# Kernel tuning notes

Measured on AMD Instinct MI355X. Metric: run time of the kernel, lower is better.

Reference implementation:

```python
import jax, jax.numpy as jnp
import numpy as np

B, T, C, I = 4, 4096, 1024, 4096

def rmsnorm(x, w, eps=1e-6):
    return x * jax.lax.rsqrt(jnp.mean(x * x, axis=-1, keepdims=True) + eps) * w

def shift(h):
    # prepend zeros, drop last timestep: (B,T,C)
    return jnp.pad(h, ((0, 0), (1, 0), (0, 0)))[:, :-1]

def wkv_scan(k, v, w, u):
    # k, v: (B,T,C) fp32; w, u: (C,)
    ew = jnp.exp(jnp.clip(w, -20.0, 20.0))
    def step(carry, kv):
        a, b = carry
        kt, vt = kv  # (B,C)
        ekt = jnp.exp(jnp.clip(u + kt, -20.0, 20.0))
        out = (a + ekt * vt) / (b + ekt + 1e-8)
        ek = jnp.exp(jnp.clip(kt, -20.0, 20.0))
        return (ew * a + ek * vt, ew * b + ek), out
    init = (jnp.zeros((k.shape[0], k.shape[2]), jnp.float32),
            jnp.zeros((k.shape[0], k.shape[2]), jnp.float32))
    _, out = jax.lax.scan(step, init, (k.swapaxes(0, 1), v.swapaxes(0, 1)))
    return out.swapaxes(0, 1)  # (B,T,C)

def setup_inputs() -> dict:
    key = jax.random.key(0)
    ks = jax.random.split(key, 16)
    s = 1.0 / np.sqrt(C)
    si = 1.0 / np.sqrt(I)
    return {
        "x": jax.random.normal(ks[0], (B, T, C), jnp.float32),
        "ln1_w": jnp.ones((C,), jnp.float32),
        "ln2_w": jnp.ones((C,), jnp.float32),
        "time_decay": jax.random.normal(ks[1], (C,), jnp.float32) * 0.1 - 5.0,
        "time_first": jax.random.normal(ks[2], (C,), jnp.float32) * 0.01,
        "time_mix_k": jnp.full((C,), 0.5, jnp.float32),
        "time_mix_v": jnp.full((C,), 0.5, jnp.float32),
        "time_mix_r": jnp.full((C,), 0.5, jnp.float32),
        "W_key": jax.random.normal(ks[3], (C, C), jnp.float32) * s,
        "W_value": jax.random.normal(ks[4], (C, C), jnp.float32) * s,
        "W_recept": jax.random.normal(ks[5], (C, C), jnp.float32) * s,
        "W_out": jax.random.normal(ks[6], (C, C), jnp.float32) * s,
        "time_mix_k2": jnp.full((C,), 0.5, jnp.float32),
        "time_mix_r2": jnp.full((C,), 0.5, jnp.float32),
        "W_key2": jax.random.normal(ks[7], (C, I), jnp.float32) * s,
        "W_value2": jax.random.normal(ks[8], (I, C), jnp.float32) * si,
        "W_recept2": jax.random.normal(ks[9], (C, C), jnp.float32) * s,
    }

def reference(x, ln1_w, ln2_w, time_decay, time_first,
              time_mix_k, time_mix_v, time_mix_r,
              W_key, W_value, W_recept, W_out,
              time_mix_k2, time_mix_r2, W_key2, W_value2, W_recept2):
    # --- time mixing ---
    h = rmsnorm(x, ln1_w)
    sh = shift(h)
    xk = h * time_mix_k + sh * (1 - time_mix_k)
    xv = h * time_mix_v + sh * (1 - time_mix_v)
    xr = h * time_mix_r + sh * (1 - time_mix_r)
    k = xk @ W_key
    v = xv @ W_value
    r = jax.nn.sigmoid(xr @ W_recept)
    w = -jnp.exp(time_decay)
    u = time_first
    wkv = wkv_scan(k.astype(jnp.float32), v.astype(jnp.float32), w, u).astype(x.dtype)
    x = x + (r * wkv) @ W_out
    # --- channel mixing ---
    h = rmsnorm(x, ln2_w)
    sh = shift(h)
    xk = h * time_mix_k2 + sh * (1 - time_mix_k2)
    xr = h * time_mix_r2 + sh * (1 - time_mix_r2)
    k2 = jnp.square(jax.nn.relu(xk @ W_key2))
    r2 = jax.nn.sigmoid(xr @ W_recept2)
    return x + r2 * (k2 @ W_value2)
```

## Files before the change

kernel.cpp:

```cpp
#include <hip/hip_runtime.h>
#include <cstdint>
#include <cstddef>

#define B_ 4
#define T_ 4096
#define C_ 1024
#define I_ 4096
#define M_ (B_*T_)

__device__ __forceinline__ float bf2f(uint16_t u) {
    union { uint32_t i; float f; } v; v.i = ((uint32_t)u) << 16; return v.f;
}
__device__ __forceinline__ uint16_t f2bf(float f) {
    union { float f; uint32_t i; } v; v.f = f;
    uint32_t i = v.i;
    return (uint16_t)((i + 0x7fffu + ((i >> 16) & 1u)) >> 16);
}

typedef __bf16 bf16x8 __attribute__((ext_vector_type(8)));
typedef float  f32x4  __attribute__((ext_vector_type(4)));
typedef uint32_t u32x4 __attribute__((ext_vector_type(4)));

__device__ __forceinline__ void async16(const void* g, void* l) {
    __builtin_amdgcn_global_load_lds(
        (const __attribute__((address_space(1))) void*)g,
        (__attribute__((address_space(3))) void*)l, 16, 0, 0);
}

#define MEMBAR asm volatile("" ::: "memory")
#define BAR    __builtin_amdgcn_s_barrier()

__global__ void sniff_kernel(const uint32_t* __restrict__ w,
                             int* __restrict__ flag, int* __restrict__ one) {
    *flag = (w[0] == 0x3F003F00u) ? 1 : 0;
    *one = 1;
}

struct VecPtrs { const void* s[9]; uint16_t* d[9]; };
__global__ __launch_bounds__(256) void convert_vecs(VecPtrs p, const int* __restrict__ flagp) {
    const int f = *flagp;
    const int tid = threadIdx.x;
    for (int a = 0; a < 9; ++a) {
        const void* s = p.s[a]; uint16_t* d = p.d[a];
        for (int i = tid; i < C_; i += 256)
            d[i] = f ? ((const uint16_t*)s)[i] : f2bf(((const float*)s)[i]);
    }
}

struct TJobs { const void* src[7]; uint16_t* dst[7]; };
__global__ __launch_bounds__(256) void transpose_all(TJobs tj, const int* __restrict__ flagp)
{
    __shared__ uint16_t tile[64][65];
    const int f = *flagp;
    const int bid = blockIdx.x;
    int w, t, R, Cc, cx, cy;
    if (bid < 1280) {
        w = bid >> 8; t = bid & 255; R = C_; Cc = C_; cx = t & 15; cy = t >> 4;
    } else if (bid < 2304) {
        w = 5; t = bid - 1280; R = C_; Cc = I_; cx = t & 63; cy = t >> 6;
    } else {
        w = 6; t = bid - 2304; R = I_; Cc = C_; cx = t & 15; cy = t >> 4;
    }
    const void* in = tj.src[w];
    uint16_t* out = tj.dst[w];
    const int lc = threadIdx.x & 63;
    const int rg = threadIdx.x >> 6;
    const int c0 = cx * 64, r0 = cy * 64;
    #pragma unroll
    for (int i = 0; i < 16; ++i) {
        int lr = rg * 16 + i;
        size_t idx = (size_t)(r0 + lr) * Cc + c0 + lc;
        tile[lr][lc] = f ? ((const uint16_t*)in)[idx] : f2bf(((const float*)in)[idx]);
    }
    __syncthreads();
    #pragma unroll
    for (int i = 0; i < 16; ++i) {
        int lcc = rg * 16 + i;
        out[(size_t)(c0 + lcc) * R + r0 + lc] = tile[lc][lcc];
    }
}

__global__ __launch_bounds__(256) void mix_kernel(
    const void* __restrict__ x, const uint16_t* __restrict__ ln,
    const uint16_t* __restrict__ mk, const uint16_t* __restrict__ mv,
    const uint16_t* __restrict__ mr, const int* __restrict__ flagp,
    uint16_t* __restrict__ xk, uint16_t* __restrict__ xv, uint16_t* __restrict__ xr)
{
    const int row = blockIdx.x;
    const int tid = threadIdx.x;
    const int f = *flagp;
    const bool hasPrev = (row & (T_ - 1)) != 0;
    const size_t base = (size_t)row * C_;

    float c[4], p[4];
    if (f) {
        const uint16_t* xb = (const uint16_t*)x;
        uint2 cu = ((const uint2*)(xb + base))[tid];
        uint2 pu; pu.x = 0u; pu.y = 0u;
        if (hasPrev) pu = ((const uint2*)(xb + base - C_))[tid];
        c[0] = bf2f((uint16_t)(cu.x & 0xffff)); c[1] = bf2f((uint16_t)(cu.x >> 16));
        c[2] = bf2f((uint16_t)(cu.y & 0xffff)); c[3] = bf2f((uint16_t)(cu.y >> 16));
        p[0] = bf2f((uint16_t)(pu.x & 0xffff)); p[1] = bf2f((uint16_t)(pu.x >> 16));
        p[2] = bf2f((uint16_t)(pu.y & 0xffff)); p[3] = bf2f((uint16_t)(pu.y >> 16));
    } else {
        const float* xf = (const float*)x;
        float4 cf = ((const float4*)(xf + base))[tid];
        float4 pf; pf.x = pf.y = pf.z = pf.w = 0.f;
        if (hasPrev) pf = ((const float4*)(xf + base - C_))[tid];
        c[0] = cf.x; c[1] = cf.y; c[2] = cf.z; c[3] = cf.w;
        p[0] = pf.x; p[1] = pf.y; p[2] = pf.z; p[3] = pf.w;
    }

    float s1 = c[0]*c[0] + c[1]*c[1] + c[2]*c[2] + c[3]*c[3];
    float s2 = p[0]*p[0] + p[1]*p[1] + p[2]*p[2] + p[3]*p[3];
    #pragma unroll
    for (int off = 32; off > 0; off >>= 1) {
        s1 += __shfl_down(s1, off);
        s2 += __shfl_down(s2, off);
    }
    __shared__ float red[8];
    const int lane = tid & 63, wave = tid >> 6;
    if (lane == 0) { red[wave * 2] = s1; red[wave * 2 + 1] = s2; }
    __syncthreads();
    s1 = red[0] + red[2] + red[4] + red[6];
    s2 = red[1] + red[3] + red[5] + red[7];
    const float rs1 = rsqrtf(s1 * (1.f / C_) + 1e-6f);
    const float rs2 = rsqrtf(s2 * (1.f / C_) + 1e-6f);

    uint2 lnu = ((const uint2*)ln)[tid];
    uint2 mku = ((const uint2*)mk)[tid];
    uint2 mru = ((const uint2*)mr)[tid];
    float lnv[4] = { bf2f((uint16_t)(lnu.x & 0xffff)), bf2f((uint16_t)(lnu.x >> 16)),
                     bf2f((uint16_t)(lnu.y & 0xffff)), bf2f((uint16_t)(lnu.y >> 16)) };
    float mkv[4] = { bf2f((uint16_t)(mku.x & 0xffff)), bf2f((uint16_t)(mku.x >> 16)),
                     bf2f((uint16_t)(mku.y & 0xffff)), bf2f((uint16_t)(mku.y >> 16)) };
    float mrv[4] = { bf2f((uint16_t)(mru.x & 0xffff)), bf2f((uint16_t)(mru.x >> 16)),
                     bf2f((uint16_t)(mru.y & 0xffff)), bf2f((uint16_t)(mru.y >> 16)) };

    float h[4], sh[4];
    #pragma unroll
    for (int e = 0; e < 4; ++e) {
        h[e]  = c[e] * rs1 * lnv[e];
        sh[e] = p[e] * rs2 * lnv[e];
    }

    uint16_t ok[4], orr[4];
    #pragma unroll
    for (int e = 0; e < 4; ++e) {
        ok[e]  = f2bf(h[e] * mkv[e] + sh[e] * (1.f - mkv[e]));
        orr[e] = f2bf(h[e] * mrv[e] + sh[e] * (1.f - mrv[e]));
    }
    uint2 w;
    w.x = (uint32_t)ok[0] | ((uint32_t)ok[1] << 16);  w.y = (uint32_t)ok[2] | ((uint32_t)ok[3] << 16);
    ((uint2*)(xk + base))[tid] = w;
    w.x = (uint32_t)orr[0] | ((uint32_t)orr[1] << 16); w.y = (uint32_t)orr[2] | ((uint32_t)orr[3] << 16);
    ((uint2*)(xr + base))[tid] = w;

    if (xv != nullptr) {
        uint2 mvu = ((const uint2*)mv)[tid];
        float mvv[4] = { bf2f((uint16_t)(mvu.x & 0xffff)), bf2f((uint16_t)(mvu.x >> 16)),
                         bf2f((uint16_t)(mvu.y & 0xffff)), bf2f((uint16_t)(mvu.y >> 16)) };
        uint16_t ov[4];
        #pragma unroll
        for (int e = 0; e < 4; ++e)
            ov[e] = f2bf(h[e] * mvv[e] + sh[e] * (1.f - mvv[e]));
        w.x = (uint32_t)ov[0] | ((uint32_t)ov[1] << 16);  w.y = (uint32_t)ov[2] | ((uint32_t)ov[3] << 16);
        ((uint2*)(xv + base))[tid] = w;
    }
}

#define SCAN_L   64
#define SCAN_NCH (T_ / SCAN_L)

__global__ __launch_bounds__(256) void wkv_pass1(
    const uint16_t* __restrict__ kb, const uint16_t* __restrict__ vb,
    const uint16_t* __restrict__ td,
    float* __restrict__ sumA, float* __restrict__ sumB)
{
    const int gid = blockIdx.x * 256 + threadIdx.x;
    const int c = gid & (C_ - 1);
    const int j = (gid >> 10) & (SCAN_NCH - 1);
    const int b = gid >> 16;
    float w = -__expf(bf2f(td[c]));
    w = fminf(fmaxf(w, -20.f), 20.f);
    const float ew = __expf(w);
    const size_t base = ((size_t)(b * T_ + j * SCAN_L)) * C_ + c;
    float A = 0.f, Bs = 0.f;
    #pragma unroll 8
    for (int i = 0; i < SCAN_L; ++i) {
        float kt = bf2f(kb[base + (size_t)i * C_]);
        float vt = bf2f(vb[base + (size_t)i * C_]);
        float ek = __expf(fminf(fmaxf(kt, -20.f), 20.f));
        A  = ew * A  + ek * vt;
        Bs = ew * Bs + ek;
    }
    const size_t sidx = ((size_t)(b * SCAN_NCH + j)) * C_ + c;
    sumA[sidx] = A; sumB[sidx] = Bs;
}

__global__ __launch_bounds__(256) void wkv_pass2(
    const float* __restrict__ sumA, const float* __restrict__ sumB,
    const uint16_t* __restrict__ td,
    float* __restrict__ a0s, float* __restrict__ b0s)
{
    const int gid = blockIdx.x * 256 + threadIdx.x;
    const int c = gid & (C_ - 1);
    const int b = gid >> 10;
    float w = -__expf(bf2f(td[c]));
    w = fminf(fmaxf(w, -20.f), 20.f);
    const float dL = __expf(w * (float)SCAN_L);
    float a = 0.f, bs = 0.f;
    for (int j = 0; j < SCAN_NCH; ++j) {
        size_t idx = ((size_t)(b * SCAN_NCH + j)) * C_ + c;
        a0s[idx] = a; b0s[idx] = bs;
        a  = dL * a  + sumA[idx];
        bs = dL * bs + sumB[idx];
    }
}

__global__ __launch_bounds__(256) void wkv_pass3(
    const uint16_t* __restrict__ kb, const uint16_t* __restrict__ vb,
    const uint16_t* __restrict__ rb, const uint16_t* __restrict__ td,
    const uint16_t* __restrict__ tf,
    const float* __restrict__ a0s, const float* __restrict__ b0s,
    uint16_t* __restrict__ rwkv)
{
    const int gid = blockIdx.x * 256 + threadIdx.x;
    const int c = gid & (C_ - 1);
    const int j = (gid >> 10) & (SCAN_NCH - 1);
    const int b = gid >> 16;
    float w = -__expf(bf2f(td[c]));
    w = fminf(fmaxf(w, -20.f), 20.f);
    const float ew = __expf(w);
    const float u = bf2f(tf[c]);
    const size_t base = ((size_t)(b * T_ + j * SCAN_L)) * C_ + c;
    const size_t sidx = ((size_t)(b * SCAN_NCH + j)) * C_ + c;
    float a = a0s[sidx], bs = b0s[sidx];
    #pragma unroll 4
    for (int i = 0; i < SCAN_L; ++i) {
        float kt = bf2f(kb[base + (size_t)i * C_]);
        float vt = bf2f(vb[base + (size_t)i * C_]);
        float rt = bf2f(rb[base + (size_t)i * C_]);
        float eu = __expf(fminf(fmaxf(u + kt, -20.f), 20.f));
        float out = __fdividef(a + eu * vt, bs + eu + 1e-8f);
        rwkv[base + (size_t)i * C_] = f2bf(rt * out);
        float ek = __expf(fminf(fmaxf(kt, -20.f), 20.f));
        a  = ew * a  + ek * vt;
        bs = ew * bs + ek;
    }
}


struct GJob {
    const uint16_t* A; const uint16_t* BT; void* Out;
    const void* aux1; const void* aux2;
    int mode; int N; int K;
};
struct GJobs { GJob j[3]; };

#define EP_PITCH 72
#define EP_QUAD  4608

#define MFMA_QUAD(RB)                                                         \
    _Pragma("unroll")                                                         \
    for (int ii = 0; ii < 4; ++ii) {                                          \
        _Pragma("unroll")                                                     \
        for (int jj = 0; jj < 4; ++jj)                                        \
            acc[(RB) + ii][jj] = __builtin_amdgcn_mfma_f32_16x16x32_bf16(     \
                av[ii], bv[jj], acc[(RB) + ii][jj], 0, 0, 0);                 \
    }

__device__ __forceinline__ void gemm_loop256(
    const uint16_t* __restrict__ Abase, const uint16_t* __restrict__ Bbase,
    const int K, uint16_t* __restrict__ sA, uint16_t* __restrict__ sB,
    const int tid, const int aOff, const int bOff, f32x4 (&acc)[8][4])
{
    const int r0  = tid >> 2;
    const int kg8 = ((tid & 3) ^ ((r0 >> 1) & 3)) * 8;
    const uint16_t* gA = Abase + (size_t)r0 * K + kg8;
    const uint16_t* gB = Bbase + (size_t)r0 * K + kg8;
    uint16_t* dA = sA + tid * 8;
    uint16_t* dB = sB + tid * 8;
    const size_t qs = (size_t)128 * K;
    const int NT = K >> 6;

    async16(gA,      dA);         async16(gA + qs,      dA + 4096);
    async16(gB,      dB);         async16(gB + qs,      dB + 4096);
    async16(gA + 32, dA + 8192);  async16(gA + 32 + qs, dA + 12288);
    async16(gB + 32, dB + 8192);  async16(gB + 32 + qs, dB + 12288);
    asm volatile("s_waitcnt vmcnt(4)" ::: "memory");
    BAR; MEMBAR;

    for (int t = 0; t < NT; ++t) {
        const int s0 = (t & 1) * 2;
        const int n0 = s0 ^ 2;
        const uint16_t* A0 = sA + s0 * 8192 + aOff;
        const uint16_t* B0 = sB + s0 * 8192 + bOff;
        const uint16_t* A1 = A0 + 8192;
        const uint16_t* B1 = B0 + 8192;
        uint16_t* dAn = dA + n0 * 8192;
        uint16_t* dBn = dB + n0 * 8192;
        const bool pf = (t + 1 < NT);
        const int ko = (t + 1) << 6;
        bf16x8 av[4], bv[4];

        #pragma unroll
        for (int ii = 0; ii < 4; ++ii) av[ii] = *(const bf16x8*)(A0 + ii * 512);
        #pragma unroll
        for (int jj = 0; jj < 4; ++jj) bv[jj] = *(const bf16x8*)(B0 + jj * 512);
        if (pf) {
            async16(gA + ko,      dAn);          async16(gA + ko + qs,      dAn + 4096);
            async16(gB + ko,      dBn);          async16(gB + ko + qs,      dBn + 4096);
            async16(gA + ko + 32, dAn + 8192);   async16(gA + ko + 32 + qs, dAn + 12288);
            async16(gB + ko + 32, dBn + 8192);   async16(gB + ko + 32 + qs, dBn + 12288);
        }
        MEMBAR;
        BAR; MEMBAR;
        __builtin_amdgcn_s_setprio(1);
        MFMA_QUAD(0)
        __builtin_amdgcn_s_setprio(0);
        BAR; MEMBAR;

        #pragma unroll
        for (int ii = 0; ii < 4; ++ii) av[ii] = *(const bf16x8*)(A0 + 2048 + ii * 512);
        if (pf) asm volatile("s_waitcnt vmcnt(8)" ::: "memory");
        else    asm volatile("s_waitcnt vmcnt(0)" ::: "memory");
        BAR; MEMBAR;
        __builtin_amdgcn_s_setprio(1);
        MFMA_QUAD(4)
        __builtin_amdgcn_s_setprio(0);
        BAR; MEMBAR;

        #pragma unroll
        for (int ii = 0; ii < 4; ++ii) av[ii] = *(const bf16x8*)(A1 + ii * 512);
        #pragma unroll
        for (int jj = 0; jj < 4; ++jj) bv[jj] = *(const bf16x8*)(B1 + jj * 512);
        MEMBAR;
        BAR; MEMBAR;
        __builtin_amdgcn_s_setprio(1);
        MFMA_QUAD(0)
        __builtin_amdgcn_s_setprio(0);
        BAR; MEMBAR;

        #pragma unroll
        for (int ii = 0; ii < 4; ++ii) av[ii] = *(const bf16x8*)(A1 + 2048 + ii * 512);
        if (pf) asm volatile("s_waitcnt vmcnt(4)" ::: "memory");
        BAR; MEMBAR;
        __builtin_amdgcn_s_setprio(1);
        MFMA_QUAD(4)
        __builtin_amdgcn_s_setprio(0);
        BAR; MEMBAR;
    }
}

__global__ __launch_bounds__(512, 2) void gemm256(GJobs js, const int* __restrict__ flagp)
{
    __shared__ uint16_t smem[65536];
    uint16_t* sA = smem;
    uint16_t* sB = smem + 32768;

    const GJob jb = js.j[blockIdx.z];
    const int N = jb.N, K = jb.K, mode = jb.mode;
    const int tid = threadIdx.x;
    const int lane = tid & 63, wave = tid >> 6;
    const int laneM = lane & 15, quad = lane >> 4;
    const int wm = wave >> 2, wn = wave & 3;

    const int nwg = gridDim.x;
    const int nPN = nwg >> 6;
    const int xcd = blockIdx.x & 7;
    const int local = blockIdx.x >> 3;
    const int stCol = (nPN >= 4) ? (nPN >> 2) : 1;
    const int st = local >> 4;
    const int within = local & 15;
    const int spm = within & 3, spn = within >> 2;
    const int stc = st % stCol, str = st / stCol;
    const int pm = xcd * 8 + str * 4 + spm;
    const int pn = stc * 4 + spn;
    const int tileM = pm << 8, tileN = pn << 8;

    const int slot8 = (quad ^ ((laneM >> 1) & 3)) * 8;
    const int aOff = (wm * 128 + laneM) * 32 + slot8;
    const int bOff = (wn * 64  + laneM) * 32 + slot8;

    f32x4 acc[8][4];
    #pragma unroll
    for (int i = 0; i < 8; ++i)
        #pragma unroll
        for (int j = 0; j < 4; ++j)
            acc[i][j] = (f32x4){0.f, 0.f, 0.f, 0.f};

    gemm_loop256(jb.A + (size_t)tileM * K, jb.BT + (size_t)tileN * K,
                 K, sA, sB, tid, aOff, bOff, acc);

    const int f = (mode == 2 || mode == 4) ? *flagp : 1;

    #pragma unroll
    for (int h = 0; h < 2; ++h) {
        if (h) __syncthreads();
        #pragma unroll
        for (int ii = 0; ii < 4; ++ii) {
            #pragma unroll
            for (int jj = 0; jj < 4; ++jj) {
                #pragma unroll
                for (int rr = 0; rr < 4; ++rr) {
                    float v = acc[h * 4 + ii][jj][rr];
                    if (mode == 1) v = __fdividef(1.f, 1.f + __expf(-v));
                    else if (mode == 3) { float tt = fmaxf(v, 0.f); v = tt * tt; }
                    smem[wave * EP_QUAD + (ii * 16 + quad * 4 + rr) * EP_PITCH
                         + jj * 16 + laneM] = f2bf(v);
                }
            }
        }
        __syncthreads();
        #pragma unroll
        for (int s = 0; s < 8; ++s) {
            int segid = s * 512 + tid;
            int gr = segid >> 5;
            int c0 = (segid & 31) * 8;
            int band = gr >> 6, lr = gr & 63;
            int lidx = (band * 4 + (c0 >> 6)) * EP_QUAD + lr * EP_PITCH + (c0 & 63);
            u32x4 pk = *(const u32x4*)&smem[lidx];
            size_t idx = (size_t)(tileM + band * 128 + h * 64 + lr) * N + tileN + c0;

            if (mode == 2) {
                union { u32x4 u; uint16_t hh[8]; } P; P.u = pk;
                float xres[8];
                if (f) {
                    union { u32x4 u; uint16_t hh[8]; } A1u;
                    A1u.u = __builtin_nontemporal_load(
                        (const u32x4*)((const uint16_t*)jb.aux1 + idx));
                    #pragma unroll
                    for (int e = 0; e < 8; ++e) xres[e] = bf2f(A1u.hh[e]);
                } else {
                    const float* af = (const float*)jb.aux1 + idx;
                    f32x4 a0 = __builtin_nontemporal_load((const f32x4*)af);
                    f32x4 a1 = __builtin_nontemporal_load((const f32x4*)(af + 4));
                    #pragma unroll
                    for (int e = 0; e < 4; ++e) { xres[e] = a0[e]; xres[e + 4] = a1[e]; }
                }
                union { u32x4 u; uint16_t hh[8]; } O;
                #pragma unroll
                for (int e = 0; e < 8; ++e) O.hh[e] = f2bf(bf2f(P.hh[e]) + xres[e]);
                __builtin_nontemporal_store(O.u, (u32x4*)((uint16_t*)jb.Out + idx));
            } else if (mode == 4) {
                union { u32x4 u; uint16_t hh[8]; } P, X, R;
                P.u = pk;
                X.u = __builtin_nontemporal_load(
                    (const u32x4*)((const uint16_t*)jb.aux1 + idx));
                R.u = __builtin_nontemporal_load(
                    (const u32x4*)((const uint16_t*)jb.aux2 + idx));
                float res[8];
                #pragma unroll
                for (int e = 0; e < 8; ++e)
                    res[e] = bf2f(X.hh[e]) + bf2f(R.hh[e]) * bf2f(P.hh[e]);
                if (f) {
                    union { u32x4 u; uint16_t hh[8]; } O;
                    #pragma unroll
                    for (int e = 0; e < 8; ++e) O.hh[e] = f2bf(res[e]);
                    __builtin_nontemporal_store(O.u, (u32x4*)((uint16_t*)jb.Out + idx));
                } else {
                    float* of = (float*)jb.Out + idx;
                    f32x4 o0, o1;
                    o0[0]=res[0]; o0[1]=res[1]; o0[2]=res[2]; o0[3]=res[3];
                    o1[0]=res[4]; o1[1]=res[5]; o1[2]=res[6]; o1[3]=res[7];
                    __builtin_nontemporal_store(o0, (f32x4*)of);
                    __builtin_nontemporal_store(o1, (f32x4*)(of + 4));
                }
            } else {
                __builtin_nontemporal_store(pk, (u32x4*)((uint16_t*)jb.Out + idx));
            }
        }
    }
}

extern "C" void kernel_launch(void* const* d_in, const int* in_sizes, int n_in,
                              void* d_out, int out_size, void* d_ws, size_t ws_size,
                              hipStream_t stream)
{
    const void* x   = d_in[0];
    const void* ln1 = d_in[1];
    const void* ln2 = d_in[2];
    const void* td  = d_in[3];
    const void* tf  = d_in[4];
    const void* mk  = d_in[5];
    const void* mv  = d_in[6];
    const void* mr  = d_in[7];
    const void* Wk  = d_in[8];
    const void* Wv  = d_in[9];
    const void* Wr  = d_in[10];
    const void* Wo  = d_in[11];
    const void* mk2 = d_in[12];
    const void* mr2 = d_in[13];
    const void* Wk2 = d_in[14];
    const void* Wv2 = d_in[15];
    const void* Wr2 = d_in[16];

    char* ws = (char*)d_ws;
    const size_t MiB = 1u << 20;
    uint16_t* WkT  = (uint16_t*)(ws + 0 * MiB);
    uint16_t* WvT  = (uint16_t*)(ws + 2 * MiB);
    uint16_t* WrT  = (uint16_t*)(ws + 4 * MiB);
    uint16_t* WoT  = (uint16_t*)(ws + 6 * MiB);
    uint16_t* Wr2T = (uint16_t*)(ws + 8 * MiB);
    uint16_t* Wk2T = (uint16_t*)(ws + 10 * MiB);
    uint16_t* Wv2T = (uint16_t*)(ws + 18 * MiB);
    uint16_t* A0 = (uint16_t*)(ws + 26 * MiB);
    uint16_t* A1 = (uint16_t*)(ws + 58 * MiB);
    uint16_t* A2 = (uint16_t*)(ws + 90 * MiB);
    uint16_t* A3 = (uint16_t*)(ws + 122 * MiB);
    uint16_t* A4 = (uint16_t*)(ws + 154 * MiB);
    uint16_t* A5 = (uint16_t*)(ws + 186 * MiB);
    uint16_t* k2 = (uint16_t*)(ws + 122 * MiB);
    float* sumA = (float*)(ws + 58 * MiB);
    float* sumB = (float*)(ws + 59 * MiB);
    float* a0s  = (float*)(ws + 60 * MiB);
    float* b0s  = (float*)(ws + 61 * MiB);
    int* flagp = (int*)(ws + 250 * MiB);
    int* onep  = (int*)(ws + 250 * MiB + 16);
    uint16_t* vecs = (uint16_t*)(ws + 250 * MiB + 64);
    uint16_t* ln1c = vecs + 0 * C_;
    uint16_t* ln2c = vecs + 1 * C_;
    uint16_t* tdc  = vecs + 2 * C_;
    uint16_t* tfc  = vecs + 3 * C_;
    uint16_t* mkc  = vecs + 4 * C_;
    uint16_t* mvc  = vecs + 5 * C_;
    uint16_t* mrc  = vecs + 6 * C_;
    uint16_t* mk2c = vecs + 7 * C_;
    uint16_t* mr2c = vecs + 8 * C_;

    uint16_t* xk   = A0;
    uint16_t* xv   = A1;
    uint16_t* xr   = A2;
    uint16_t* kb   = A3;
    uint16_t* vb   = A4;
    uint16_t* rb   = A5;
    uint16_t* rwkv = A0;
    uint16_t* x2   = A1;
    uint16_t* xk2  = A2;
    uint16_t* xr2  = A0;
    uint16_t* r2   = A2;

    dim3 blk(256);

    sniff_kernel<<<1, 1, 0, stream>>>((const uint32_t*)mk, flagp, onep);
    VecPtrs vp;
    vp.s[0] = ln1; vp.s[1] = ln2; vp.s[2] = td;  vp.s[3] = tf;  vp.s[4] = mk;
    vp.s[5] = mv;  vp.s[6] = mr;  vp.s[7] = mk2; vp.s[8] = mr2;
    vp.d[0] = ln1c; vp.d[1] = ln2c; vp.d[2] = tdc;  vp.d[3] = tfc;  vp.d[4] = mkc;
    vp.d[5] = mvc;  vp.d[6] = mrc;  vp.d[7] = mk2c; vp.d[8] = mr2c;
    convert_vecs<<<1, blk, 0, stream>>>(vp, flagp);

    TJobs tj;
    tj.src[0] = Wk;  tj.dst[0] = WkT;
    tj.src[1] = Wv;  tj.dst[1] = WvT;
    tj.src[2] = Wr;  tj.dst[2] = WrT;
    tj.src[3] = Wo;  tj.dst[3] = WoT;
    tj.src[4] = Wr2; tj.dst[4] = Wr2T;
    tj.src[5] = Wk2; tj.dst[5] = Wk2T;
    tj.src[6] = Wv2; tj.dst[6] = Wv2T;
    transpose_all<<<3328, blk, 0, stream>>>(tj, flagp);

    mix_kernel<<<M_, blk, 0, stream>>>(x, ln1c, mkc, mvc, mrc, flagp, xk, xv, xr);

    GJobs kvr;
    kvr.j[0] = GJob{ xk, WkT, kb, nullptr, nullptr, 0, C_, C_ };
    kvr.j[1] = GJob{ xv, WvT, vb, nullptr, nullptr, 0, C_, C_ };
    kvr.j[2] = GJob{ xr, WrT, rb, nullptr, nullptr, 1, C_, C_ };
    gemm256<<<dim3(64 * (C_ >> 8), 1, 3), 512, 0, stream>>>(kvr, flagp);

    wkv_pass1<<<(B_ * SCAN_NCH * C_) / 256, blk, 0, stream>>>(kb, vb, tdc, sumA, sumB);
    wkv_pass2<<<(B_ * C_) / 256, blk, 0, stream>>>(sumA, sumB, tdc, a0s, b0s);
    wkv_pass3<<<(B_ * SCAN_NCH * C_) / 256, blk, 0, stream>>>(kb, vb, rb, tdc, tfc, a0s, b0s, rwkv);

    GJobs g2; g2.j[0] = GJob{ rwkv, WoT, x2, x, nullptr, 2, C_, C_ };
    g2.j[1] = g2.j[0]; g2.j[2] = g2.j[0];
    gemm256<<<dim3(64 * (C_ >> 8), 1, 1), 512, 0, stream>>>(g2, flagp);

    mix_kernel<<<M_, blk, 0, stream>>>(x2, ln2c, mk2c, nullptr, mr2c, onep, xk2, nullptr, xr2);

    GJobs g3; g3.j[0] = GJob{ xk2, Wk2T, k2, nullptr, nullptr, 3, I_, C_ };
    g3.j[1] = g3.j[0]; g3.j[2] = g3.j[0];
    gemm256<<<dim3(64 * (I_ >> 8), 1, 1), 512, 0, stream>>>(g3, flagp);

    GJobs g4a; g4a.j[0] = GJob{ xr2, Wr2T, r2, nullptr, nullptr, 1, C_, C_ };
    g4a.j[1] = g4a.j[0]; g4a.j[2] = g4a.j[0];
    gemm256<<<dim3(64 * (C_ >> 8), 1, 1), 512, 0, stream>>>(g4a, flagp);

    GJobs g4b; g4b.j[0] = GJob{ k2, Wv2T, d_out, x2, r2, 4, C_, I_ };
    g4b.j[1] = g4b.j[0]; g4b.j[2] = g4b.j[0];
    gemm256<<<dim3(64 * (C_ >> 8), 1, 1), 512, 0, stream>>>(g4b, flagp);

    (void)in_sizes; (void)n_in; (void)out_size; (void)ws_size;
}
```

Before: 912.0 us.

## Replace 256x256 GEMM tiles with 128x128 tiles using 256-thread blocks

Every GEMM moves from a 256x256 tile with 512 threads and 128 KB of LDS to a 128x128 tile with 256 threads and 64 KB of LDS. Each wave now holds a 64x64 accumulator block, and the per-tile-K prefetch is split into two half-K phases with their own waits. The XCD-aware tile swizzle and the epilogue are rewritten for the smaller tile. The goal is more workgroups for better CU occupancy and load balance on mi355x, at the cost of lower arithmetic intensity and more global and L2 traffic per FLOP.

```diff
diff --git a/kernel.cpp b/kernel.cpp
--- a/kernel.cpp
+++ b/kernel.cpp
@@ -27,7 +27,6 @@
         (__attribute__((address_space(3))) void*)l, 16, 0, 0);
 }
 
-#define MEMBAR asm volatile("" ::: "memory")
 #define BAR    __builtin_amdgcn_s_barrier()
 
 __global__ void sniff_kernel(const uint32_t* __restrict__ w,
@@ -261,19 +260,19 @@
 #define EP_PITCH 72
 #define EP_QUAD  4608
 
-#define MFMA_QUAD(RB)                                                         \
+#define MFMA16                                                                \
     _Pragma("unroll")                                                         \
     for (int ii = 0; ii < 4; ++ii) {                                          \
         _Pragma("unroll")                                                     \
         for (int jj = 0; jj < 4; ++jj)                                        \
-            acc[(RB) + ii][jj] = __builtin_amdgcn_mfma_f32_16x16x32_bf16(     \
-                av[ii], bv[jj], acc[(RB) + ii][jj], 0, 0, 0);                 \
-    }
-
-__device__ __forceinline__ void gemm_loop256(
+            acc[ii][jj] = __builtin_amdgcn_mfma_f32_16x16x32_bf16(            \
+                av[ii], bv[jj], acc[ii][jj], 0, 0, 0);                        \
+    }
+
+__device__ __forceinline__ void gemm_loop128(
     const uint16_t* __restrict__ Abase, const uint16_t* __restrict__ Bbase,
     const int K, uint16_t* __restrict__ sA, uint16_t* __restrict__ sB,
-    const int tid, const int aOff, const int bOff, f32x4 (&acc)[8][4])
+    const int tid, const int aOff, const int bOff, f32x4 (&acc)[4][4])
 {
     const int r0  = tid >> 2;
     const int kg8 = ((tid & 3) ^ ((r0 >> 1) & 3)) * 8;
@@ -281,25 +280,25 @@
     const uint16_t* gB = Bbase + (size_t)r0 * K + kg8;
     uint16_t* dA = sA + tid * 8;
     uint16_t* dB = sB + tid * 8;
-    const size_t qs = (size_t)128 * K;
+    const size_t qs = (size_t)64 * K;
     const int NT = K >> 6;
 
-    async16(gA,      dA);         async16(gA + qs,      dA + 4096);
-    async16(gB,      dB);         async16(gB + qs,      dB + 4096);
-    async16(gA + 32, dA + 8192);  async16(gA + 32 + qs, dA + 12288);
-    async16(gB + 32, dB + 8192);  async16(gB + 32 + qs, dB + 12288);
+    async16(gA,      dA);        async16(gA + qs,      dA + 2048);
+    async16(gB,      dB);        async16(gB + qs,      dB + 2048);
+    async16(gA + 32, dA + 4096); async16(gA + 32 + qs, dA + 6144);
+    async16(gB + 32, dB + 4096); async16(gB + 32 + qs, dB + 6144);
     asm volatile("s_waitcnt vmcnt(4)" ::: "memory");
-    BAR; MEMBAR;
+    BAR;
 
     for (int t = 0; t < NT; ++t) {
         const int s0 = (t & 1) * 2;
         const int n0 = s0 ^ 2;
-        const uint16_t* A0 = sA + s0 * 8192 + aOff;
-        const uint16_t* B0 = sB + s0 * 8192 + bOff;
-        const uint16_t* A1 = A0 + 8192;
-        const uint16_t* B1 = B0 + 8192;
-        uint16_t* dAn = dA + n0 * 8192;
-        uint16_t* dBn = dB + n0 * 8192;
+        const uint16_t* A0 = sA + s0 * 4096 + aOff;
+        const uint16_t* B0 = sB + s0 * 4096 + bOff;
+        const uint16_t* A1 = A0 + 4096;
+        const uint16_t* B1 = B0 + 4096;
+        uint16_t* dAn = dA + n0 * 4096;
+        uint16_t* dBn = dB + n0 * 4096;
         const bool pf = (t + 1 < NT);
         const int ko = (t + 1) << 6;
         bf16x8 av[4], bv[4];
@@ -309,167 +308,147 @@
         #pragma unroll
         for (int jj = 0; jj < 4; ++jj) bv[jj] = *(const bf16x8*)(B0 + jj * 512);
         if (pf) {
-            async16(gA + ko,      dAn);          async16(gA + ko + qs,      dAn + 4096);
-            async16(gB + ko,      dBn);          async16(gB + ko + qs,      dBn + 4096);
-            async16(gA + ko + 32, dAn + 8192);   async16(gA + ko + 32 + qs, dAn + 12288);
-            async16(gB + ko + 32, dBn + 8192);   async16(gB + ko + 32 + qs, dBn + 12288);
+            async16(gA + ko, dAn);  async16(gA + ko + qs, dAn + 2048);
+            async16(gB + ko, dBn);  async16(gB + ko + qs, dBn + 2048);
         }
-        MEMBAR;
-        BAR; MEMBAR;
+        if (pf) asm volatile("s_waitcnt vmcnt(4)" ::: "memory");
+        else    asm volatile("s_waitcnt vmcnt(0)" ::: "memory");
+        BAR;
         __builtin_amdgcn_s_setprio(1);
-        MFMA_QUAD(0)
+        MFMA16
         __builtin_amdgcn_s_setprio(0);
-        BAR; MEMBAR;
-
-        #pragma unroll
-        for (int ii = 0; ii < 4; ++ii) av[ii] = *(const bf16x8*)(A0 + 2048 + ii * 512);
-        if (pf) asm volatile("s_waitcnt vmcnt(8)" ::: "memory");
+        BAR;
+
+        #pragma unroll
+        for (int ii = 0; ii < 4; ++ii) av[ii] = *(const bf16x8*)(A1 + ii * 512);
+        #pragma unroll
+        for (int jj = 0; jj < 4; ++jj) bv[jj] = *(const bf16x8*)(B1 + jj * 512);
+        if (pf) {
+            async16(gA + ko + 32, dAn + 4096);  async16(gA + ko + 32 + qs, dAn + 6144);
+            async16(gB + ko + 32, dBn + 4096);  async16(gB + ko + 32 + qs, dBn + 6144);
+        }
+        if (pf) asm volatile("s_waitcnt vmcnt(4)" ::: "memory");
         else    asm volatile("s_waitcnt vmcnt(0)" ::: "memory");
-        BAR; MEMBAR;
+        BAR;
         __builtin_amdgcn_s_setprio(1);
-        MFMA_QUAD(4)
+        MFMA16
         __builtin_amdgcn_s_setprio(0);
-        BAR; MEMBAR;
-
-        #pragma unroll
-        for (int ii = 0; ii < 4; ++ii) av[ii] = *(const bf16x8*)(A1 + ii * 512);
-        #pragma unroll
-        for (int jj = 0; jj < 4; ++jj) bv[jj] = *(const bf16x8*)(B1 + jj * 512);
-        MEMBAR;
-        BAR; MEMBAR;
-        __builtin_amdgcn_s_setprio(1);
-        MFMA_QUAD(0)
-        __builtin_amdgcn_s_setprio(0);
-        BAR; MEMBAR;
-
-        #pragma unroll
-        for (int ii = 0; ii < 4; ++ii) av[ii] = *(const bf16x8*)(A1 + 2048 + ii * 512);
-        if (pf) asm volatile("s_waitcnt vmcnt(4)" ::: "memory");
-        BAR; MEMBAR;
-        __builtin_amdgcn_s_setprio(1);
-        MFMA_QUAD(4)
-        __builtin_amdgcn_s_setprio(0);
-        BAR; MEMBAR;
-    }
-}
-
-__global__ __launch_bounds__(512, 2) void gemm256(GJobs js, const int* __restrict__ flagp)
-{
-    __shared__ uint16_t smem[65536];
+        BAR;
+    }
+}
+
+__global__ __launch_bounds__(256, 2) void gemm128(GJobs js, const int* __restrict__ flagp)
+{
+    __shared__ uint16_t smem[32768];
     uint16_t* sA = smem;
-    uint16_t* sB = smem + 32768;
+    uint16_t* sB = smem + 16384;
 
     const GJob jb = js.j[blockIdx.z];
     const int N = jb.N, K = jb.K, mode = jb.mode;
     const int tid = threadIdx.x;
     const int lane = tid & 63, wave = tid >> 6;
     const int laneM = lane & 15, quad = lane >> 4;
-    const int wm = wave >> 2, wn = wave & 3;
-
-    const int nwg = gridDim.x;
-    const int nPN = nwg >> 6;
+    const int wm = wave >> 1, wn = wave & 1;
+
+    const int nPN = gridDim.x >> 7;
     const int xcd = blockIdx.x & 7;
     const int local = blockIdx.x >> 3;
-    const int stCol = (nPN >= 4) ? (nPN >> 2) : 1;
+    const int within = local & 15;
     const int st = local >> 4;
-    const int within = local & 15;
+    const int stCol = nPN >> 2;
+    const int stc = st % stCol, str = st / stCol;
     const int spm = within & 3, spn = within >> 2;
-    const int stc = st % stCol, str = st / stCol;
-    const int pm = xcd * 8 + str * 4 + spm;
+    const int pm = xcd * 16 + str * 4 + spm;
     const int pn = stc * 4 + spn;
-    const int tileM = pm << 8, tileN = pn << 8;
+    const int tileM = pm << 7, tileN = pn << 7;
 
     const int slot8 = (quad ^ ((laneM >> 1) & 3)) * 8;
-    const int aOff = (wm * 128 + laneM) * 32 + slot8;
-    const int bOff = (wn * 64  + laneM) * 32 + slot8;
-
-    f32x4 acc[8][4];
-    #pragma unroll
-    for (int i = 0; i < 8; ++i)
+    const int aOff = (wm * 64 + laneM) * 32 + slot8;
+    const int bOff = (wn * 64 + laneM) * 32 + slot8;
+
+    f32x4 acc[4][4];
+    #pragma unroll
+    for (int i = 0; i < 4; ++i)
         #pragma unroll
         for (int j = 0; j < 4; ++j)
             acc[i][j] = (f32x4){0.f, 0.f, 0.f, 0.f};
 
-    gemm_loop256(jb.A + (size_t)tileM * K, jb.BT + (size_t)tileN * K,
+    gemm_loop128(jb.A + (size_t)tileM * K, jb.BT + (size_t)tileN * K,
                  K, sA, sB, tid, aOff, bOff, acc);
 
     const int f = (mode == 2 || mode == 4) ? *flagp : 1;
 
-    #pragma unroll
-    for (int h = 0; h < 2; ++h) {
-        if (h) __syncthreads();
-        #pragma unroll
-        for (int ii = 0; ii < 4; ++ii) {
+    const int qbase = (wm * 2 + wn) * EP_QUAD;
+    #pragma unroll
+    for (int ii = 0; ii < 4; ++ii) {
+        #pragma unroll
+        for (int jj = 0; jj < 4; ++jj) {
             #pragma unroll
-            for (int jj = 0; jj < 4; ++jj) {
-                #pragma unroll
-                for (int rr = 0; rr < 4; ++rr) {
-                    float v = acc[h * 4 + ii][jj][rr];
-                    if (mode == 1) v = __fdividef(1.f, 1.f + __expf(-v));
-                    else if (mode == 3) { float tt = fmaxf(v, 0.f); v = tt * tt; }
-                    smem[wave * EP_QUAD + (ii * 16 + quad * 4 + rr) * EP_PITCH
-                         + jj * 16 + laneM] = f2bf(v);
-                }
+            for (int rr = 0; rr < 4; ++rr) {
+                float v = acc[ii][jj][rr];
+                if (mode == 1) v = __fdividef(1.f, 1.f + __expf(-v));
+                else if (mode == 3) { float tt = fmaxf(v, 0.f); v = tt * tt; }
+                smem[qbase + (ii * 16 + quad * 4 + rr) * EP_PITCH + jj * 16 + laneM] = f2bf(v);
             }
         }
-        __syncthreads();
-        #pragma unroll
-        for (int s = 0; s < 8; ++s) {
-            int segid = s * 512 + tid;
-            int gr = segid >> 5;
-            int c0 = (segid & 31) * 8;
-            int band = gr >> 6, lr = gr & 63;
-            int lidx = (band * 4 + (c0 >> 6)) * EP_QUAD + lr * EP_PITCH + (c0 & 63);
-            u32x4 pk = *(const u32x4*)&smem[lidx];
-            size_t idx = (size_t)(tileM + band * 128 + h * 64 + lr) * N + tileN + c0;
-
-            if (mode == 2) {
-                union { u32x4 u; uint16_t hh[8]; } P; P.u = pk;
-                float xres[8];
-                if (f) {
-                    union { u32x4 u; uint16_t hh[8]; } A1u;
-                    A1u.u = __builtin_nontemporal_load(
-                        (const u32x4*)((const uint16_t*)jb.aux1 + idx));
-                    #pragma unroll
-                    for (int e = 0; e < 8; ++e) xres[e] = bf2f(A1u.hh[e]);
-                } else {
-                    const float* af = (const float*)jb.aux1 + idx;
-                    f32x4 a0 = __builtin_nontemporal_load((const f32x4*)af);
-                    f32x4 a1 = __builtin_nontemporal_load((const f32x4*)(af + 4));
-                    #pragma unroll
-                    for (int e = 0; e < 4; ++e) { xres[e] = a0[e]; xres[e + 4] = a1[e]; }
-                }
+    }
+    __syncthreads();
+
+    #pragma unroll
+    for (int s = 0; s < 8; ++s) {
+        int segid = s * 256 + tid;
+        int gr = segid >> 4;
+        int c0 = (segid & 15) * 8;
+        int lidx = ((gr >> 6) * 2 + (c0 >> 6)) * EP_QUAD + (gr & 63) * EP_PITCH + (c0 & 63);
+        u32x4 pk = *(const u32x4*)&smem[lidx];
+        size_t idx = (size_t)(tileM + gr) * N + tileN + c0;
+
+        if (mode == 2) {
+            union { u32x4 u; uint16_t hh[8]; } P; P.u = pk;
+            float xres[8];
+            if (f) {
+                union { u32x4 u; uint16_t hh[8]; } A1u;
+                A1u.u = __builtin_nontemporal_load(
+                    (const u32x4*)((const uint16_t*)jb.aux1 + idx));
+                #pragma unroll
+                for (int e = 0; e < 8; ++e) xres[e] = bf2f(A1u.hh[e]);
+            } else {
+                const float* af = (const float*)jb.aux1 + idx;
+                f32x4 a0 = __builtin_nontemporal_load((const f32x4*)af);
+                f32x4 a1 = __builtin_nontemporal_load((const f32x4*)(af + 4));
+                #pragma unroll
+                for (int e = 0; e < 4; ++e) { xres[e] = a0[e]; xres[e + 4] = a1[e]; }
+            }
+            union { u32x4 u; uint16_t hh[8]; } O;
+            #pragma unroll
+            for (int e = 0; e < 8; ++e) O.hh[e] = f2bf(bf2f(P.hh[e]) + xres[e]);
+            __builtin_nontemporal_store(O.u, (u32x4*)((uint16_t*)jb.Out + idx));
+        } else if (mode == 4) {
+            union { u32x4 u; uint16_t hh[8]; } P, X, R;
+            P.u = pk;
+            X.u = __builtin_nontemporal_load(
+                (const u32x4*)((const uint16_t*)jb.aux1 + idx));
+            R.u = __builtin_nontemporal_load(
+                (const u32x4*)((const uint16_t*)jb.aux2 + idx));
+            float res[8];
+            #pragma unroll
+            for (int e = 0; e < 8; ++e)
+                res[e] = bf2f(X.hh[e]) + bf2f(R.hh[e]) * bf2f(P.hh[e]);
+            if (f) {
                 union { u32x4 u; uint16_t hh[8]; } O;
                 #pragma unroll
-                for (int e = 0; e < 8; ++e) O.hh[e] = f2bf(bf2f(P.hh[e]) + xres[e]);
+                for (int e = 0; e < 8; ++e) O.hh[e] = f2bf(res[e]);
                 __builtin_nontemporal_store(O.u, (u32x4*)((uint16_t*)jb.Out + idx));
-            } else if (mode == 4) {
-                union { u32x4 u; uint16_t hh[8]; } P, X, R;
-                P.u = pk;
-                X.u = __builtin_nontemporal_load(
-                    (const u32x4*)((const uint16_t*)jb.aux1 + idx));
-                R.u = __builtin_nontemporal_load(
-                    (const u32x4*)((const uint16_t*)jb.aux2 + idx));
-                float res[8];
-                #pragma unroll
-                for (int e = 0; e < 8; ++e)
-                    res[e] = bf2f(X.hh[e]) + bf2f(R.hh[e]) * bf2f(P.hh[e]);
-                if (f) {
-                    union { u32x4 u; uint16_t hh[8]; } O;
-                    #pragma unroll
-                    for (int e = 0; e < 8; ++e) O.hh[e] = f2bf(res[e]);
-                    __builtin_nontemporal_store(O.u, (u32x4*)((uint16_t*)jb.Out + idx));
-                } else {
-                    float* of = (float*)jb.Out + idx;
-                    f32x4 o0, o1;
-                    o0[0]=res[0]; o0[1]=res[1]; o0[2]=res[2]; o0[3]=res[3];
-                    o1[0]=res[4]; o1[1]=res[5]; o1[2]=res[6]; o1[3]=res[7];
-                    __builtin_nontemporal_store(o0, (f32x4*)of);
-                    __builtin_nontemporal_store(o1, (f32x4*)(of + 4));
-                }
             } else {
-                __builtin_nontemporal_store(pk, (u32x4*)((uint16_t*)jb.Out + idx));
+                float* of = (float*)jb.Out + idx;
+                f32x4 o0, o1;
+                o0[0]=res[0]; o0[1]=res[1]; o0[2]=res[2]; o0[3]=res[3];
+                o1[0]=res[4]; o1[1]=res[5]; o1[2]=res[6]; o1[3]=res[7];
+                __builtin_nontemporal_store(o0, (f32x4*)of);
+                __builtin_nontemporal_store(o1, (f32x4*)(of + 4));
             }
+        } else {
+            __builtin_nontemporal_store(pk, (u32x4*)((uint16_t*)jb.Out + idx));
         }
     }
 }
@@ -567,7 +546,7 @@
     kvr.j[0] = GJob{ xk, WkT, kb, nullptr, nullptr, 0, C_, C_ };
     kvr.j[1] = GJob{ xv, WvT, vb, nullptr, nullptr, 0, C_, C_ };
     kvr.j[2] = GJob{ xr, WrT, rb, nullptr, nullptr, 1, C_, C_ };
-    gemm256<<<dim3(64 * (C_ >> 8), 1, 3), 512, 0, stream>>>(kvr, flagp);
+    gemm128<<<dim3(128 * (C_ >> 7), 1, 3), blk, 0, stream>>>(kvr, flagp);
 
     wkv_pass1<<<(B_ * SCAN_NCH * C_) / 256, blk, 0, stream>>>(kb, vb, tdc, sumA, sumB);
     wkv_pass2<<<(B_ * C_) / 256, blk, 0, stream>>>(sumA, sumB, tdc, a0s, b0s);
@@ -575,21 +554,21 @@
 
     GJobs g2; g2.j[0] = GJob{ rwkv, WoT, x2, x, nullptr, 2, C_, C_ };
     g2.j[1] = g2.j[0]; g2.j[2] = g2.j[0];
-    gemm256<<<dim3(64 * (C_ >> 8), 1, 1), 512, 0, stream>>>(g2, flagp);
+    gemm128<<<dim3(128 * (C_ >> 7), 1, 1), blk, 0, stream>>>(g2, flagp);
 
     mix_kernel<<<M_, blk, 0, stream>>>(x2, ln2c, mk2c, nullptr, mr2c, onep, xk2, nullptr, xr2);
 
     GJobs g3; g3.j[0] = GJob{ xk2, Wk2T, k2, nullptr, nullptr, 3, I_, C_ };
     g3.j[1] = g3.j[0]; g3.j[2] = g3.j[0];
-    gemm256<<<dim3(64 * (I_ >> 8), 1, 1), 512, 0, stream>>>(g3, flagp);
+    gemm128<<<dim3(128 * (I_ >> 7), 1, 1), blk, 0, stream>>>(g3, flagp);
 
     GJobs g4a; g4a.j[0] = GJob{ xr2, Wr2T, r2, nullptr, nullptr, 1, C_, C_ };
     g4a.j[1] = g4a.j[0]; g4a.j[2] = g4a.j[0];
-    gemm256<<<dim3(64 * (C_ >> 8), 1, 1), 512, 0, stream>>>(g4a, flagp);
+    gemm128<<<dim3(128 * (C_ >> 7), 1, 1), blk, 0, stream>>>(g4a, flagp);
 
     GJobs g4b; g4b.j[0] = GJob{ k2, Wv2T, d_out, x2, r2, 4, C_, I_ };
     g4b.j[1] = g4b.j[0]; g4b.j[2] = g4b.j[0];
-    gemm256<<<dim3(64 * (C_ >> 8), 1, 1), 512, 0, stream>>>(g4b, flagp);
+    gemm128<<<dim3(128 * (C_ >> 7), 1, 1), blk, 0, stream>>>(g4b, flagp);
 
     (void)in_sizes; (void)n_in; (void)out_size; (void)ws_size;
 }
```

After: 926.8 us. Within noise of the previous version (+1.6%).
